# Kernel tuning notes

Hardware: AMD Instinct MI355X
Metric: run time of the kernel (lower is better)

The kernel has to match this reference:

```python
import jax, jax.numpy as jnp
import numpy as np

B, D, L = 4096, 128, 4
ALPHA = 1.0
SLOPE = 0.1  # LeakyReLU negative slope


def _leaky(h):
    return jnp.where(h > 0, h, SLOPE * h)


def _dleaky(h):
    return jnp.where(h > 0, 1.0, SLOPE).astype(h.dtype)


def setup_inputs() -> dict:
    key = jax.random.key(0)
    ks = jax.random.split(key, 7)
    scale = 0.5 / np.sqrt(D)  # keep residual roughly Lipschitz < 1
    x = jax.random.normal(ks[0], (B, D), jnp.float32)
    W1 = jax.random.normal(ks[1], (L, D, D), jnp.float32) * scale
    b1 = jax.random.normal(ks[2], (L, D), jnp.float32) * 0.01
    W2 = jax.random.normal(ks[3], (L, D, D), jnp.float32) * scale
    b2 = jax.random.normal(ks[4], (L, D), jnp.float32) * 0.01
    W3 = jax.random.normal(ks[5], (L, D, D), jnp.float32) * scale
    b3 = jax.random.normal(ks[6], (L, D), jnp.float32) * 0.01
    return {"x": x, "W1": W1, "b1": b1, "W2": W2, "b2": b2, "W3": W3, "b3": b3}


def reference(x, W1, b1, W2, b2, W3, b3):
    logdet = jnp.zeros(x.shape[0], x.dtype)
    for i in range(L):  # small fixed number of structurally distinct blocks
        w1, w2, w3 = W1[i], W2[i], W3[i]
        # --- block forward: x <- x + alpha * f(x) ---
        h1 = x @ w1.T + b1[i]
        h2 = _leaky(h1) @ w2.T + b2[i]
        f = _leaky(h2) @ w3.T + b3[i]
        x = x + ALPHA * f
        # --- log|det J_f| evaluated at the NEW x (as in the original code) ---
        g1 = x @ w1.T + b1[i]          # [B, D] pre-activation 1
        d1 = _dleaky(g1)
        g2 = _leaky(g1) @ w2.T + b2[i]  # [B, D] pre-activation 2
        d2 = _dleaky(g2)
        # J[b] = w3 @ diag(d2[b]) @ w2 @ diag(d1[b]) @ w1  -> [B, D, D]
        J = (w3[None, :, :] * d2[:, None, :]) @ w2
        J = (J * d1[:, None, :]) @ w1
        s = jnp.linalg.svd(J, compute_uv=False)  # [B, D] singular values
        logdet = logdet + jnp.sum(jnp.log(s), axis=-1)
    return x, logdet
```

## Files before the change

### kernel.cpp

```cpp
#include <hip/hip_runtime.h>

typedef __attribute__((ext_vector_type(8))) short short8;
typedef __attribute__((ext_vector_type(4))) float float4f;

#define PADX 132
#define LOG_SLOPE -2.302585092994046f
#define LN2 0.6931471805599453f
#define NBLK 268

__device__ __forceinline__ float bf2f(unsigned int u) {
    return __builtin_bit_cast(float, u << 16);
}
__device__ __forceinline__ unsigned short f2bf(float f) {
    unsigned int x = __builtin_bit_cast(unsigned int, f);
    x += 0x7fff + ((x >> 16) & 1);
    return (unsigned short)(x >> 16);
}

template<int ISF32>
__device__ __forceinline__ float ldv(const void* p, int i) {
    if (ISF32) return ((const float*)p)[i];
    return bf2f(((const unsigned short*)p)[i]);
}

__device__ __forceinline__ int detect_f32(const unsigned short* W1u, int lane) {
    unsigned int u = W1u[lane * 2];
    unsigned int e = (u >> 7) & 0xFF;
    int bad = (e < 64) || (e > 135);
    return __ballot(bad) != 0ull;
}

__device__ __forceinline__ float4f mfma16(short8 a, short8 b, float4f c) {
    return __builtin_amdgcn_mfma_f32_16x16x32_bf16(a, b, c, 0, 0, 0);
}

__device__ __forceinline__ void split8(float4f a, float4f b, short8& hi, short8& lo) {
#pragma unroll
    for (int j = 0; j < 4; ++j) {
        float v = a[j]; unsigned short h = f2bf(v);
        hi[j] = (short)h; lo[j] = (short)f2bf(v - bf2f(h));
        v = b[j]; h = f2bf(v);
        hi[4 + j] = (short)h; lo[4 + j] = (short)f2bf(v - bf2f(h));
    }
}

template<int MODE, int ISF32>
__device__ __forceinline__ void matvec(const float* in, float* out,
                                       const void* __restrict__ W, int wofs,
                                       const void* __restrict__ bias, int bofs,
                                       int lane, int colb, int* cnt) {
    const int m = lane & 15, q = lane >> 4;
    const int c0 = colb + m, c1 = colb + 16 + m;
    float b0 = ldv<ISF32>(bias, bofs + c0);
    float b1v = ldv<ISF32>(bias, bofs + c1);
    float4f acc0 = {b0, b0, b0, b0};
    float4f acc1 = {b1v, b1v, b1v, b1v};
    __syncthreads();
#pragma unroll
    for (int kk = 0; kk < 4; ++kk) {
        const int kc = kk * 32 + q * 8;
        const float* xp = in + m * PADX + kc;
        short8 xh, xl;
        split8(*(const float4f*)xp, *(const float4f*)(xp + 4), xh, xl);
        if (ISF32) {
            const float* w0p = (const float*)W + wofs + c0 * 128 + kc;
            const float* w1p = (const float*)W + wofs + c1 * 128 + kc;
            short8 w0h, w0l, w1h, w1l;
            split8(*(const float4f*)w0p, *(const float4f*)(w0p + 4), w0h, w0l);
            split8(*(const float4f*)w1p, *(const float4f*)(w1p + 4), w1h, w1l);
            acc0 = mfma16(xh, w0h, acc0);
            acc0 = mfma16(xl, w0h, acc0);
            acc0 = mfma16(xh, w0l, acc0);
            acc1 = mfma16(xh, w1h, acc1);
            acc1 = mfma16(xl, w1h, acc1);
            acc1 = mfma16(xh, w1l, acc1);
        } else {
            short8 w0 = *(const short8*)((const unsigned short*)W + wofs + c0 * 128 + kc);
            short8 w1 = *(const short8*)((const unsigned short*)W + wofs + c1 * 128 + kc);
            acc0 = mfma16(xh, w0, acc0);
            acc0 = mfma16(xl, w0, acc0);
            acc1 = mfma16(xh, w1, acc1);
            acc1 = mfma16(xl, w1, acc1);
        }
    }
    __syncthreads();
    const int rbase = q * 4;
    int c[4];
#pragma unroll
    for (int r = 0; r < 4; ++r) {
        float v0 = acc0[r], v1 = acc1[r];
        int row = rbase + r;
        if (MODE == 1) {
            out[row * PADX + c0] += v0;
            out[row * PADX + c1] += v1;
        } else {
            if (MODE >= 2) c[r] = (v0 <= 0.0f) + (v1 <= 0.0f);
            if (MODE != 3) {
                out[row * PADX + c0] = v0 > 0.0f ? v0 : 0.1f * v0;
                out[row * PADX + c1] = v1 > 0.0f ? v1 : 0.1f * v1;
            }
        }
    }
    if (MODE >= 2) {
#pragma unroll
        for (int r = 0; r < 4; ++r) {
            int cc = c[r];
            cc += __shfl_xor(cc, 1);
            cc += __shfl_xor(cc, 2);
            cc += __shfl_xor(cc, 4);
            cc += __shfl_xor(cc, 8);
            if (m == 0) atomicAdd(&cnt[rbase + r], cc);
        }
    }
}

template<int ISF32>
__device__ __forceinline__ void fwd(int bid, int tid, int lane, float* lds,
        const void* x, const void* W1, const void* b1, const void* W2, const void* b2,
        const void* W3, const void* b3, void* out, float* ws) {
    const int r0 = bid * 16;
    float* X = lds;
    float* T = lds + 16 * PADX;
    int* cnt = (int*)(lds + 32 * PADX);
    for (int e = tid; e < 2048; e += 256) {
        int r = e >> 7, c = e & 127;
        X[r * PADX + c] = ldv<ISF32>(x, (r0 + r) * 128 + c);
    }
    if (tid < 16) cnt[tid] = 0;
    const int colb = (tid >> 6) * 32;
#pragma unroll 1
    for (int layer = 0; layer < 4; ++layer) {
        const int wofs = layer * 16384, bofs = layer * 128;
        matvec<0, ISF32>(X, T, W1, wofs, b1, bofs, lane, colb, cnt);
        matvec<0, ISF32>(T, T, W2, wofs, b2, bofs, lane, colb, cnt);
        matvec<1, ISF32>(T, X, W3, wofs, b3, bofs, lane, colb, cnt);
        matvec<2, ISF32>(X, T, W1, wofs, b1, bofs, lane, colb, cnt);
        matvec<3, ISF32>(T, T, W2, wofs, b2, bofs, lane, colb, cnt);
    }
    __syncthreads();
    for (int e = tid; e < 2048; e += 256) {
        int r = e >> 7, c = e & 127;
        float v = X[r * PADX + c];
        if (ISF32) ((float*)out)[(r0 + r) * 128 + c] = v;
        else ((unsigned short*)out)[(r0 + r) * 128 + c] = f2bf(v);
    }
    if (tid < 16) ws[64 + r0 + tid] = (float)cnt[tid];
}

template<int ISF32>
__device__ __forceinline__ float lu_logdet(int id, int tid, float* lds,
        const void* W1, const void* W2, const void* W3) {
    const int wsel = id % 3;
    const void* Wm = (wsel == 0 ? W1 : (wsel == 1 ? W2 : W3));
    const int ofs = (id / 3) * 16384;
    const int tx = tid & 31, ty = tid >> 5;
    float* rowbuf = lds;
    float* colbuf = lds + 256;
    float4f V[16];
#pragma unroll
    for (int m = 0; m < 16; ++m) {
        int base = ofs + (ty + 8 * m) * 128 + 4 * tx;
        if (ISF32) {
            V[m] = *(const float4f*)((const float*)Wm + base);
        } else {
            ushort4 u = *(const ushort4*)((const unsigned short*)Wm + base);
            V[m] = (float4f){bf2f(u.x), bf2f(u.y), bf2f(u.z), bf2f(u.w)};
        }
    }
    if (ty == 0) *(float4f*)&rowbuf[4 * tx] = V[0];
    if (tx == 0) {
#pragma unroll
        for (int m = 0; m < 16; ++m) colbuf[ty * 16 + m] = V[m][0];
    }
    __syncthreads();
    float logacc = 0.0f;
    for (int k = 0; k < 128; ++k) {
        const int buf = (k & 1) << 7;
        float akk = rowbuf[buf + k];
        float4f rk = *(const float4f*)&rowbuf[buf + 4 * tx];
        float G[16];
        *(float4f*)&G[0]  = *(const float4f*)&colbuf[buf + ty * 16];
        *(float4f*)&G[4]  = *(const float4f*)&colbuf[buf + ty * 16 + 4];
        *(float4f*)&G[8]  = *(const float4f*)&colbuf[buf + ty * 16 + 8];
        *(float4f*)&G[12] = *(const float4f*)&colbuf[buf + ty * 16 + 12];
        float rp = 1.0f / akk;
        logacc += __log2f(fabsf(akk));
#pragma unroll
        for (int m = 0; m < 16; ++m) {
            int r = ty + 8 * m;
            float gg = (r > k) ? G[m] * rp : 0.0f;
            V[m][0] -= gg * rk[0]; V[m][1] -= gg * rk[1];
            V[m][2] -= gg * rk[2]; V[m][3] -= gg * rk[3];
        }
        if (k < 127) {
            const int nk = k + 1;
            const int nbuf = (nk & 1) << 7;
            if (ty == (nk & 7)) {
                float4f* dst = (float4f*)&rowbuf[nbuf + 4 * tx];
                switch (nk >> 3) {
                case 0:  *dst = V[0];  break;
                case 1:  *dst = V[1];  break;
                case 2:  *dst = V[2];  break;
                case 3:  *dst = V[3];  break;
                case 4:  *dst = V[4];  break;
                case 5:  *dst = V[5];  break;
                case 6:  *dst = V[6];  break;
                case 7:  *dst = V[7];  break;
                case 8:  *dst = V[8];  break;
                case 9:  *dst = V[9];  break;
                case 10: *dst = V[10]; break;
                case 11: *dst = V[11]; break;
                case 12: *dst = V[12]; break;
                case 13: *dst = V[13]; break;
                case 14: *dst = V[14]; break;
                default: *dst = V[15]; break;
                }
            }
            if (tx == (nk >> 2)) {
                switch (nk & 3) {
                case 0:
#pragma unroll
                    for (int m = 0; m < 16; ++m) colbuf[nbuf + ty * 16 + m] = V[m][0];
                    break;
                case 1:
#pragma unroll
                    for (int m = 0; m < 16; ++m) colbuf[nbuf + ty * 16 + m] = V[m][1];
                    break;
                case 2:
#pragma unroll
                    for (int m = 0; m < 16; ++m) colbuf[nbuf + ty * 16 + m] = V[m][2];
                    break;
                default:
#pragma unroll
                    for (int m = 0; m < 16; ++m) colbuf[nbuf + ty * 16 + m] = V[m][3];
                }
            }
        }
        __syncthreads();
    }
    return logacc * LN2;
}

__global__ __launch_bounds__(256) void k_main(
        const void* __restrict__ x,
        const void* __restrict__ W1, const void* __restrict__ b1,
        const void* __restrict__ W2, const void* __restrict__ b2,
        const void* __restrict__ W3, const void* __restrict__ b3,
        void* __restrict__ out, float* __restrict__ ws) {
    __shared__ float lds[16384];
    __shared__ int s_last;
    const int tid = threadIdx.x;
    const int lane = tid & 63;
    const int isf32 = detect_f32((const unsigned short*)W1, lane);

    if (blockIdx.x < 12) {
        float ld = isf32 ? lu_logdet<1>(blockIdx.x, tid, lds, W1, W2, W3)
                         : lu_logdet<0>(blockIdx.x, tid, lds, W1, W2, W3);
        if (tid == 0) ws[2 + blockIdx.x] = ld;
    } else {
        const int bid = blockIdx.x - 12;
        if (isf32) fwd<1>(bid, tid, lane, lds, x, W1, b1, W2, b2, W3, b3, out, ws);
        else       fwd<0>(bid, tid, lane, lds, x, W1, b1, W2, b2, W3, b3, out, ws);
    }

    __threadfence();
    if (tid == 0) s_last = (atomicAdd((int*)ws, 1) == NBLK - 1);
    __syncthreads();
    if (!s_last) return;
    __threadfence();
    float s = 0.0f;
#pragma unroll
    for (int i = 0; i < 12; ++i) s += ws[2 + i];
    for (int b = tid; b < 4096; b += 256) {
        float v = s + LOG_SLOPE * ws[64 + b];
        if (isf32) ((float*)out)[524288 + b] = v;
        else ((unsigned short*)out)[524288 + b] = f2bf(v);
    }
}

extern "C" void kernel_launch(void* const* d_in, const int* in_sizes, int n_in,
                              void* d_out, int out_size, void* d_ws, size_t ws_size,
                              hipStream_t stream) {
    const void* x  = d_in[0];
    const void* W1 = d_in[1];
    const void* b1 = d_in[2];
    const void* W2 = d_in[3];
    const void* b2 = d_in[4];
    const void* W3 = d_in[5];
    const void* b3 = d_in[6];
    float* ws = (float*)d_ws;

    hipMemsetAsync(d_ws, 0, 8, stream);
    hipLaunchKernelGGL(k_main, dim3(NBLK), dim3(256), 0, stream,
                       x, W1, b1, W2, b2, W3, b3, d_out, ws);
}
```

Measured before the change: 148.9 us.

## Pre-split weights into bf16 hi/lo planes and keep activations split in LDS

A new prep kernel converts W1/W2/W3 once per call into bf16 hi/lo planes in workspace, converts the biases to f32, and zeroes the counter, replacing the memset. The forward blocks now read pre-split weights directly and keep activations in LDS as bf16 hi/lo pairs. This removes the repeated float-to-bf16 splitting of both weights and activations inside every matvec. LDS per block drops from 64 KB to about 17.5 KB, which may allow more resident blocks. The costs are an extra kernel launch, extra workspace traffic, and per-matvec re-splitting of outputs; the LU path now relies on the smaller LDS buffer being large enough.

```diff
diff --git a/kernel.cpp b/kernel.cpp
--- a/kernel.cpp
+++ b/kernel.cpp
@@ -3,10 +3,13 @@
 typedef __attribute__((ext_vector_type(8))) short short8;
 typedef __attribute__((ext_vector_type(4))) float float4f;
 
-#define PADX 132
+#define PITCH 136
 #define LOG_SLOPE -2.302585092994046f
 #define LN2 0.6931471805599453f
 #define NBLK 268
+#define WS_BIAS 4160
+#define WS_WPLANES 8192
+#define NWELEM 196608
 
 __device__ __forceinline__ float bf2f(unsigned int u) {
     return __builtin_bit_cast(float, u << 16);
@@ -44,44 +47,69 @@
     }
 }
 
-template<int MODE, int ISF32>
-__device__ __forceinline__ void matvec(const float* in, float* out,
-                                       const void* __restrict__ W, int wofs,
-                                       const void* __restrict__ bias, int bofs,
+__global__ void k_prep(const void* __restrict__ W1, const void* __restrict__ W2,
+                       const void* __restrict__ W3, const void* __restrict__ b1,
+                       const void* __restrict__ b2, const void* __restrict__ b3,
+                       float* __restrict__ ws) {
+    const int tid = threadIdx.x, bid = blockIdx.x;
+    const int isf32 = detect_f32((const unsigned short*)W1, tid & 63);
+    unsigned short* whi = (unsigned short*)(ws + WS_WPLANES);
+    unsigned short* wlo = whi + NWELEM;
+    if (bid < 96) {
+        int s = (bid * 256 + tid) * 8;
+        int mat = s >> 14, off = s & 16383;
+        int wsel = mat >> 2;
+        const void* Wm = wsel == 0 ? W1 : (wsel == 1 ? W2 : W3);
+        int src = (mat & 3) * 16384 + off;
+        short8 hi, lo;
+        if (isf32) {
+            const float* p = (const float*)Wm + src;
+            split8(*(const float4f*)p, *(const float4f*)(p + 4), hi, lo);
+        } else {
+            hi = *(const short8*)((const unsigned short*)Wm + src);
+            lo = (short8){0, 0, 0, 0, 0, 0, 0, 0};
+        }
+        *(short8*)(whi + s) = hi;
+        *(short8*)(wlo + s) = lo;
+    } else {
+        for (int e = tid; e < 1536; e += 256) {
+            int bsel = e >> 9, idx = e & 511;
+            const void* bp = bsel == 0 ? b1 : (bsel == 1 ? b2 : b3);
+            ws[WS_BIAS + e] = isf32 ? ((const float*)bp)[idx]
+                                    : bf2f(((const unsigned short*)bp)[idx]);
+        }
+        if (tid == 0) ((int*)ws)[0] = 0;
+    }
+}
+
+template<int MODE>
+__device__ __forceinline__ void matvec(const unsigned short* inh, const unsigned short* inl,
+                                       unsigned short* outh, unsigned short* outl,
+                                       const unsigned short* __restrict__ whi,
+                                       const unsigned short* __restrict__ wlo,
+                                       const float* __restrict__ bias,
                                        int lane, int colb, int* cnt) {
     const int m = lane & 15, q = lane >> 4;
     const int c0 = colb + m, c1 = colb + 16 + m;
-    float b0 = ldv<ISF32>(bias, bofs + c0);
-    float b1v = ldv<ISF32>(bias, bofs + c1);
+    float b0 = bias[c0], b1v = bias[c1];
     float4f acc0 = {b0, b0, b0, b0};
     float4f acc1 = {b1v, b1v, b1v, b1v};
     __syncthreads();
 #pragma unroll
     for (int kk = 0; kk < 4; ++kk) {
         const int kc = kk * 32 + q * 8;
-        const float* xp = in + m * PADX + kc;
-        short8 xh, xl;
-        split8(*(const float4f*)xp, *(const float4f*)(xp + 4), xh, xl);
-        if (ISF32) {
-            const float* w0p = (const float*)W + wofs + c0 * 128 + kc;
-            const float* w1p = (const float*)W + wofs + c1 * 128 + kc;
-            short8 w0h, w0l, w1h, w1l;
-            split8(*(const float4f*)w0p, *(const float4f*)(w0p + 4), w0h, w0l);
-            split8(*(const float4f*)w1p, *(const float4f*)(w1p + 4), w1h, w1l);
-            acc0 = mfma16(xh, w0h, acc0);
-            acc0 = mfma16(xl, w0h, acc0);
-            acc0 = mfma16(xh, w0l, acc0);
-            acc1 = mfma16(xh, w1h, acc1);
-            acc1 = mfma16(xl, w1h, acc1);
-            acc1 = mfma16(xh, w1l, acc1);
-        } else {
-            short8 w0 = *(const short8*)((const unsigned short*)W + wofs + c0 * 128 + kc);
-            short8 w1 = *(const short8*)((const unsigned short*)W + wofs + c1 * 128 + kc);
-            acc0 = mfma16(xh, w0, acc0);
-            acc0 = mfma16(xl, w0, acc0);
-            acc1 = mfma16(xh, w1, acc1);
-            acc1 = mfma16(xl, w1, acc1);
-        }
+        short8 xh = *(const short8*)(inh + m * PITCH + kc);
+        short8 xl = *(const short8*)(inl + m * PITCH + kc);
+        short8 w0h = *(const short8*)(whi + c0 * 128 + kc);
+        short8 w1h = *(const short8*)(whi + c1 * 128 + kc);
+        short8 w0l = *(const short8*)(wlo + c0 * 128 + kc);
+        short8 w1l = *(const short8*)(wlo + c1 * 128 + kc);
+        acc0 = mfma16(xh, w0h, acc0);
+        acc0 = mfma16(xl, w0h, acc0);
+        acc0 = mfma16(xh, w0l, acc0);
+        acc1 = mfma16(xh, w1h, acc1);
+        acc1 = mfma16(xl, w1h, acc1);
+        acc1 = mfma16(xh, w1l, acc1);
     }
     __syncthreads();
     const int rbase = q * 4;
@@ -90,15 +118,21 @@
     for (int r = 0; r < 4; ++r) {
         float v0 = acc0[r], v1 = acc1[r];
         int row = rbase + r;
+        int o0 = row * PITCH + c0, o1 = row * PITCH + c1;
         if (MODE == 1) {
-            out[row * PADX + c0] += v0;
-            out[row * PADX + c1] += v1;
-        } else {
-            if (MODE >= 2) c[r] = (v0 <= 0.0f) + (v1 <= 0.0f);
-            if (MODE != 3) {
-                out[row * PADX + c0] = v0 > 0.0f ? v0 : 0.1f * v0;
-                out[row * PADX + c1] = v1 > 0.0f ? v1 : 0.1f * v1;
-            }
+            v0 += bf2f(outh[o0]) + bf2f(outl[o0]);
+            v1 += bf2f(outh[o1]) + bf2f(outl[o1]);
+        }
+        if (MODE >= 2) c[r] = (v0 <= 0.0f) + (v1 <= 0.0f);
+        if (MODE == 0 || MODE == 2) {
+            v0 = v0 > 0.0f ? v0 : 0.1f * v0;
+            v1 = v1 > 0.0f ? v1 : 0.1f * v1;
+        }
+        if (MODE != 3) {
+            unsigned short h0 = f2bf(v0);
+            outh[o0] = h0; outl[o0] = f2bf(v0 - bf2f(h0));
+            unsigned short h1 = f2bf(v1);
+            outh[o1] = h1; outl[o1] = f2bf(v1 - bf2f(h1));
         }
     }
     if (MODE >= 2) {
@@ -115,36 +149,52 @@
 }
 
 template<int ISF32>
-__device__ __forceinline__ void fwd(int bid, int tid, int lane, float* lds,
-        const void* x, const void* W1, const void* b1, const void* W2, const void* b2,
-        const void* W3, const void* b3, void* out, float* ws) {
+__device__ __forceinline__ void fwd(int bid, int tid, int lane, char* ldsb,
+                                    const void* x, const float* ws, void* out,
+                                    float* wsw) {
+    unsigned short* Xh = (unsigned short*)ldsb;
+    unsigned short* Xl = Xh + 16 * PITCH;
+    unsigned short* Th = Xl + 16 * PITCH;
+    unsigned short* Tl = Th + 16 * PITCH;
+    int* cnt = (int*)(Tl + 16 * PITCH);
+    const unsigned short* whi = (const unsigned short*)(ws + WS_WPLANES);
+    const unsigned short* wlo = whi + NWELEM;
+    const float* bias = ws + WS_BIAS;
     const int r0 = bid * 16;
-    float* X = lds;
-    float* T = lds + 16 * PADX;
-    int* cnt = (int*)(lds + 32 * PADX);
     for (int e = tid; e < 2048; e += 256) {
         int r = e >> 7, c = e & 127;
-        X[r * PADX + c] = ldv<ISF32>(x, (r0 + r) * 128 + c);
+        float v = ldv<ISF32>(x, (r0 + r) * 128 + c);
+        unsigned short h = f2bf(v);
+        Xh[r * PITCH + c] = h;
+        Xl[r * PITCH + c] = f2bf(v - bf2f(h));
     }
     if (tid < 16) cnt[tid] = 0;
     const int colb = (tid >> 6) * 32;
 #pragma unroll 1
     for (int layer = 0; layer < 4; ++layer) {
-        const int wofs = layer * 16384, bofs = layer * 128;
-        matvec<0, ISF32>(X, T, W1, wofs, b1, bofs, lane, colb, cnt);
-        matvec<0, ISF32>(T, T, W2, wofs, b2, bofs, lane, colb, cnt);
-        matvec<1, ISF32>(T, X, W3, wofs, b3, bofs, lane, colb, cnt);
-        matvec<2, ISF32>(X, T, W1, wofs, b1, bofs, lane, colb, cnt);
-        matvec<3, ISF32>(T, T, W2, wofs, b2, bofs, lane, colb, cnt);
+        const unsigned short* w1h = whi + (0 + layer) * 16384;
+        const unsigned short* w1l = wlo + (0 + layer) * 16384;
+        const unsigned short* w2h = whi + (4 + layer) * 16384;
+        const unsigned short* w2l = wlo + (4 + layer) * 16384;
+        const unsigned short* w3h = whi + (8 + layer) * 16384;
+        const unsigned short* w3l = wlo + (8 + layer) * 16384;
+        const float* b1p = bias + layer * 128;
+        const float* b2p = bias + 512 + layer * 128;
+        const float* b3p = bias + 1024 + layer * 128;
+        matvec<0>(Xh, Xl, Th, Tl, w1h, w1l, b1p, lane, colb, cnt);
+        matvec<0>(Th, Tl, Th, Tl, w2h, w2l, b2p, lane, colb, cnt);
+        matvec<1>(Th, Tl, Xh, Xl, w3h, w3l, b3p, lane, colb, cnt);
+        matvec<2>(Xh, Xl, Th, Tl, w1h, w1l, b1p, lane, colb, cnt);
+        matvec<3>(Th, Tl, Th, Tl, w2h, w2l, b2p, lane, colb, cnt);
     }
     __syncthreads();
     for (int e = tid; e < 2048; e += 256) {
         int r = e >> 7, c = e & 127;
-        float v = X[r * PADX + c];
+        float v = bf2f(Xh[r * PITCH + c]) + bf2f(Xl[r * PITCH + c]);
         if (ISF32) ((float*)out)[(r0 + r) * 128 + c] = v;
         else ((unsigned short*)out)[(r0 + r) * 128 + c] = f2bf(v);
     }
-    if (tid < 16) ws[64 + r0 + tid] = (float)cnt[tid];
+    if (tid < 16) wsw[64 + r0 + tid] = (float)cnt[tid];
 }
 
 template<int ISF32>
@@ -247,20 +297,20 @@
         const void* __restrict__ W2, const void* __restrict__ b2,
         const void* __restrict__ W3, const void* __restrict__ b3,
         void* __restrict__ out, float* __restrict__ ws) {
-    __shared__ float lds[16384];
+    __shared__ __align__(16) char ldsb[17536];
     __shared__ int s_last;
     const int tid = threadIdx.x;
     const int lane = tid & 63;
     const int isf32 = detect_f32((const unsigned short*)W1, lane);
 
     if (blockIdx.x < 12) {
-        float ld = isf32 ? lu_logdet<1>(blockIdx.x, tid, lds, W1, W2, W3)
-                         : lu_logdet<0>(blockIdx.x, tid, lds, W1, W2, W3);
+        float ld = isf32 ? lu_logdet<1>(blockIdx.x, tid, (float*)ldsb, W1, W2, W3)
+                         : lu_logdet<0>(blockIdx.x, tid, (float*)ldsb, W1, W2, W3);
         if (tid == 0) ws[2 + blockIdx.x] = ld;
     } else {
         const int bid = blockIdx.x - 12;
-        if (isf32) fwd<1>(bid, tid, lane, lds, x, W1, b1, W2, b2, W3, b3, out, ws);
-        else       fwd<0>(bid, tid, lane, lds, x, W1, b1, W2, b2, W3, b3, out, ws);
+        if (isf32) fwd<1>(bid, tid, lane, ldsb, x, ws, out, ws);
+        else       fwd<0>(bid, tid, lane, ldsb, x, ws, out, ws);
     }
 
     __threadfence();
@@ -290,7 +340,8 @@
     const void* b3 = d_in[6];
     float* ws = (float*)d_ws;
 
-    hipMemsetAsync(d_ws, 0, 8, stream);
+    hipLaunchKernelGGL(k_prep, dim3(97), dim3(256), 0, stream,
+                       W1, W2, W3, b1, b2, b3, ws);
     hipLaunchKernelGGL(k_main, dim3(NBLK), dim3(256), 0, stream,
                        x, W1, b1, W2, b2, W3, b3, d_out, ws);
 }
```

Measured after the change: 152.3 us. 1.02x slower.
